# Kernel tuning notes

Measured on AMD Instinct MI355X. Metric: run time of the kernel, lower is better.

## Reference

```python
import jax, jax.numpy as jnp
import numpy as np

TEMPERATURE = 0.1
NEGATIVE_WEIGHT = 1.0
NORM_EPS = 1e-12  # matches torch F.normalize clamp_min eps


def setup_inputs() -> dict:
    key = jax.random.key(0)
    x = jax.random.normal(key, (8, 128, 16, 8, 8), dtype=jnp.float32)
    return {"x": x}


def reference(x):
    B, F, T, H, W = x.shape
    # transpose(0,1).flatten(1).transpose(0,1): (B,F,T,H,W) -> (N, F), N = B*T*H*W
    feats = jnp.transpose(x, (1, 0, 2, 3, 4)).reshape(F, -1).T  # [N, F]
    norms = jnp.maximum(jnp.linalg.norm(feats, axis=1, keepdims=True), NORM_EPS)
    x_norm = feats / norms  # unit vectors, [N, F]
    sims = (x_norm @ x_norm.T) / TEMPERATURE  # [N, N] cosine similarities
    n = sims.shape[0]
    # masked_select(~eye) + logsumexp == logsumexp with diagonal set to -inf
    sims = jnp.where(jnp.eye(n, dtype=bool), -jnp.inf, sims)
    diversity_loss = jax.nn.logsumexp(sims)
    return NEGATIVE_WEIGHT * diversity_loss
```

## Files before the change

kernel.cpp:

```cpp
#include <hip/hip_runtime.h>
#include <hip/hip_fp8.h>
#include <math.h>


#define NTILE 8256
#define NPBLK 1376

typedef __attribute__((ext_vector_type(4))) float f32x4;

#if __has_builtin(__builtin_amdgcn_exp2f)
#define EXP2F(x) __builtin_amdgcn_exp2f(x)
#else
#define EXP2F(x) exp2f(x)
#endif

__device__ inline unsigned int pk_fp8(float f0, float f1, float f2, float f3) {
#if __has_builtin(__builtin_amdgcn_cvt_pk_fp8_f32)
    unsigned int r = 0;
    r = __builtin_amdgcn_cvt_pk_fp8_f32(f0, f1, r, false);
    r = __builtin_amdgcn_cvt_pk_fp8_f32(f2, f3, r, true);
    return r;
#else
    union { unsigned char b[4]; unsigned int u; } v;
    v.b[0] = __hip_fp8_e4m3(f0).__x; v.b[1] = __hip_fp8_e4m3(f1).__x;
    v.b[2] = __hip_fp8_e4m3(f2).__x; v.b[3] = __hip_fp8_e4m3(f3).__x;
    return v.u;
#endif
}

__global__ __launch_bounds__(256)
void normalize_kernel(const float* __restrict__ x, unsigned char* __restrict__ Xs) {
    __shared__ float ldsf[128][33];
    __shared__ float ssred[8][32];
    __shared__ float invs[32];
    const int tid = threadIdx.x;
    const int b  = blockIdx.x >> 5;
    const int r0 = (blockIdx.x & 31) * 32;
    const int rl = tid & 31, fp = tid >> 5;
    const float* px = x + b * 131072 + r0 + rl;
    float ss = 0.f;
#pragma unroll
    for (int j = 0; j < 16; ++j) {
        int f = fp * 16 + j;
        float v = px[f * 1024];
        ldsf[f][rl] = v;
        ss = fmaf(v, v, ss);
    }
    ssred[fp][rl] = ss;
    __syncthreads();
    if (tid < 32) {
        float s = 0.f;
#pragma unroll
        for (int k = 0; k < 8; ++k) s += ssred[k][tid];
        invs[tid] = 1.0f / fmaxf(sqrtf(s), 1e-12f);
    }
    __syncthreads();
    {
        const int c   = tid;
        const int rgl = c >> 7;
        const int cc  = c & 127;
        const int t8  = (cc >> 6) & 1, q = (cc >> 4) & 3, r = cc & 15;
        const int row = rgl * 16 + r;
        const float inv = invs[row];
        union { unsigned int w[4]; int4 v; } u;
#pragma unroll
        for (int half = 0; half < 2; ++half) {
            const int k0 = t8 * 64 + half * 32 + q * 8;
            u.w[half * 2 + 0] = pk_fp8(ldsf[k0 + 0][row] * inv, ldsf[k0 + 1][row] * inv,
                                       ldsf[k0 + 2][row] * inv, ldsf[k0 + 3][row] * inv);
            u.w[half * 2 + 1] = pk_fp8(ldsf[k0 + 4][row] * inv, ldsf[k0 + 5][row] * inv,
                                       ldsf[k0 + 6][row] * inv, ldsf[k0 + 7][row] * inv);
        }
        const int rgg = blockIdx.x * 2 + rgl;
        ((int4*)Xs)[rgg * 128 + cc] = u.v;
    }
}

__global__ __launch_bounds__(256, 4)
void gram_lse_kernel(const int4* __restrict__ Xs, float* __restrict__ partials) {
    const int bk = blockIdx.x;
    const int tid = threadIdx.x;
    const int lane = tid & 63, w = tid >> 6;
    const int ga = (w & 1) * 2;
    const int gb = (w >> 1) * 2;
    const int quad = lane >> 4, colL = lane & 15;
    const float C = 14.426950408889634f;

    int L = bk * 6, I0 = 0;
    while (L >= 128 - I0) { L -= 128 - I0; ++I0; }
    int Is[6], Js[6];
    {
        int ii = I0, jj = I0 + L;
#pragma unroll
        for (int s = 0; s < 6; ++s) {
            Is[s] = ii; Js[s] = jj;
            if (++jj == 128) { ++ii; jj = ii; }
        }
    }

    int4 av[2][2];
    int IcurA = Is[0];
#pragma unroll
    for (int g = 0; g < 2; ++g)
#pragma unroll
        for (int t8 = 0; t8 < 2; ++t8)
            av[g][t8] = Xs[(Is[0] * 4 + ga + g) * 128 + t8 * 64 + lane];

    int4 bv[3][2][2];
#pragma unroll
    for (int pf = 0; pf < 2; ++pf)
#pragma unroll
        for (int g = 0; g < 2; ++g)
#pragma unroll
            for (int t8 = 0; t8 < 2; ++t8)
                bv[pf][g][t8] = Xs[(Js[pf] * 4 + gb + g) * 128 + t8 * 64 + lane];

    float wsum = 0.f;
#pragma unroll
    for (int s = 0; s < 6; ++s) {
        if (s + 2 < 6) {
#pragma unroll
            for (int g = 0; g < 2; ++g)
#pragma unroll
                for (int t8 = 0; t8 < 2; ++t8)
                    bv[(s + 2) % 3][g][t8] =
                        Xs[(Js[s + 2] * 4 + gb + g) * 128 + t8 * 64 + lane];
        }
        if (Is[s] != IcurA) {
#pragma unroll
            for (int g = 0; g < 2; ++g)
#pragma unroll
                for (int t8 = 0; t8 < 2; ++t8)
                    av[g][t8] = Xs[(Is[s] * 4 + ga + g) * 128 + t8 * 64 + lane];
            IcurA = Is[s];
        }

        f32x4 acc[2][2];
#pragma unroll
        for (int i = 0; i < 2; ++i)
#pragma unroll
            for (int j = 0; j < 2; ++j) acc[i][j] = (f32x4){0.f, 0.f, 0.f, 0.f};
#pragma unroll
        for (int t = 0; t < 4; ++t) {
            long aL[2], bL[2];
#pragma unroll
            for (int g = 0; g < 2; ++g) {
                aL[g] = ((const long*)&av[g][t >> 1])[t & 1];
                bL[g] = ((const long*)&bv[s % 3][g][t >> 1])[t & 1];
            }
#pragma unroll
            for (int i = 0; i < 2; ++i)
#pragma unroll
                for (int j = 0; j < 2; ++j)
                    acc[i][j] = __builtin_amdgcn_mfma_f32_16x16x32_fp8_fp8(
                        aL[i], bL[j], acc[i][j], 0, 0, 0);
        }

        const bool diagT = (Is[s] == Js[s]);
        float lsum = 0.f;
#pragma unroll
        for (int i = 0; i < 2; ++i) {
            const int rbase = (ga + i) * 16 + quad * 4;
#pragma unroll
            for (int j = 0; j < 2; ++j) {
                const int cbase = (gb + j) * 16 + colL;
#pragma unroll
                for (int g = 0; g < 4; ++g) {
                    if (diagT && (rbase + g == cbase)) continue;
                    lsum += EXP2F(fmaf(C, acc[i][j][g], -C));
                }
            }
        }
        wsum += diagT ? lsum : 2.0f * lsum;
    }

#pragma unroll
    for (int o = 32; o > 0; o >>= 1) wsum += __shfl_down(wsum, o, 64);
    __shared__ float red[4];
    if (lane == 0) red[w] = wsum;
    __syncthreads();
    if (tid == 0) partials[bk] = red[0] + red[1] + red[2] + red[3];
}

__global__ __launch_bounds__(256)
void final_kernel(const float* __restrict__ partials, float* __restrict__ out) {
    double s = 0.0;
    for (int i = threadIdx.x; i < NPBLK; i += 256) s += (double)partials[i];
#pragma unroll
    for (int o = 32; o > 0; o >>= 1) s += __shfl_down(s, o, 64);
    __shared__ double red[4];
    if ((threadIdx.x & 63) == 0) red[threadIdx.x >> 6] = s;
    __syncthreads();
    if (threadIdx.x == 0)
        out[0] = (float)(10.0 + log(red[0] + red[1] + red[2] + red[3]));
}

extern "C" void kernel_launch(void* const* d_in, const int* in_sizes, int n_in,
                              void* d_out, int out_size, void* d_ws, size_t ws_size,
                              hipStream_t stream) {
    const float* x = (const float*)d_in[0];
    float* out = (float*)d_out;
    float* partials = (float*)d_ws;
    unsigned char* Xs = (unsigned char*)d_ws + 131072;

    normalize_kernel<<<256, 256, 0, stream>>>(x, Xs);
    gram_lse_kernel<<<NPBLK, 256, 0, stream>>>((const int4*)Xs, partials);
    final_kernel<<<1, 256, 0, stream>>>(partials, out);
}
```

Baseline: 72.06 us.

## Fuse final reduction into gram kernel via last-block atomic counter and rebalance tiles

```diff
diff --git a/kernel.cpp b/kernel.cpp
--- a/kernel.cpp
+++ b/kernel.cpp
@@ -4,7 +4,7 @@
 
 
 #define NTILE 8256
-#define NPBLK 1376
+#define NPBLK 1024
 
 typedef __attribute__((ext_vector_type(4))) float f32x4;
 
@@ -29,7 +29,9 @@
 }
 
 __global__ __launch_bounds__(256)
-void normalize_kernel(const float* __restrict__ x, unsigned char* __restrict__ Xs) {
+void normalize_kernel(const float* __restrict__ x, unsigned char* __restrict__ Xs,
+                      unsigned int* __restrict__ counter) {
+    if (blockIdx.x == 0 && threadIdx.x == 0) counter[0] = 0u;
     __shared__ float ldsf[128][33];
     __shared__ float ssred[8][32];
     __shared__ float invs[32];
@@ -76,25 +78,26 @@
     }
 }
 
-__global__ __launch_bounds__(256, 4)
-void gram_lse_kernel(const int4* __restrict__ Xs, float* __restrict__ partials) {
-    const int bk = blockIdx.x;
-    const int tid = threadIdx.x;
-    const int lane = tid & 63, w = tid >> 6;
+template <int NT>
+__device__ __forceinline__ float gram_tiles(const int4* __restrict__ Xs,
+                                            int tstart, int lane, int w) {
     const int ga = (w & 1) * 2;
     const int gb = (w >> 1) * 2;
     const int quad = lane >> 4, colL = lane & 15;
     const float C = 14.426950408889634f;
 
-    int L = bk * 6, I0 = 0;
-    while (L >= 128 - I0) { L -= 128 - I0; ++I0; }
-    int Is[6], Js[6];
+    int Is[NT], Js[NT];
     {
-        int ii = I0, jj = I0 + L;
-#pragma unroll
-        for (int s = 0; s < 6; ++s) {
-            Is[s] = ii; Js[s] = jj;
-            if (++jj == 128) { ++ii; jj = ii; }
+        const int t = tstart;
+        int i = (int)((257.0 - sqrt(66049.0 - 8.0 * (double)t)) * 0.5);
+        if (i < 0) i = 0;
+        while ((((i + 1) * (256 - i)) >> 1) <= t) ++i;
+        while (((i * (257 - i)) >> 1) > t) --i;
+        int j = i + (t - ((i * (257 - i)) >> 1));
+#pragma unroll
+        for (int s = 0; s < NT; ++s) {
+            Is[s] = i; Js[s] = j;
+            if (++j == 128) { ++i; j = i; }
         }
     }
 
@@ -117,8 +120,8 @@
 
     float wsum = 0.f;
 #pragma unroll
-    for (int s = 0; s < 6; ++s) {
-        if (s + 2 < 6) {
+    for (int s = 0; s < NT; ++s) {
+        if (s + 2 < NT) {
 #pragma unroll
             for (int g = 0; g < 2; ++g)
 #pragma unroll
@@ -157,42 +160,63 @@
         }
 
         const bool diagT = (Is[s] == Js[s]);
-        float lsum = 0.f;
+        float l0 = 0.f, l1 = 0.f;
 #pragma unroll
         for (int i = 0; i < 2; ++i) {
             const int rbase = (ga + i) * 16 + quad * 4;
+            float lacc = 0.f;
 #pragma unroll
             for (int j = 0; j < 2; ++j) {
                 const int cbase = (gb + j) * 16 + colL;
 #pragma unroll
                 for (int g = 0; g < 4; ++g) {
                     if (diagT && (rbase + g == cbase)) continue;
-                    lsum += EXP2F(fmaf(C, acc[i][j][g], -C));
+                    lacc += EXP2F(fmaf(C, acc[i][j][g], -C));
                 }
             }
-        }
+            if (i == 0) l0 = lacc; else l1 = lacc;
+        }
+        const float lsum = l0 + l1;
         wsum += diagT ? lsum : 2.0f * lsum;
     }
+    return wsum;
+}
+
+__global__ __launch_bounds__(256, 4)
+void gram_lse_kernel(const int4* __restrict__ Xs, float* __restrict__ partials,
+                     unsigned int* __restrict__ counter, float* __restrict__ out) {
+    const int bk = blockIdx.x;
+    const int tid = threadIdx.x;
+    const int lane = tid & 63, w = tid >> 6;
+    const int tstart = bk * 8 + (bk < 64 ? bk : 64);
+
+    float wsum = (bk < 64) ? gram_tiles<9>(Xs, tstart, lane, w)
+                           : gram_tiles<8>(Xs, tstart, lane, w);
 
 #pragma unroll
     for (int o = 32; o > 0; o >>= 1) wsum += __shfl_down(wsum, o, 64);
     __shared__ float red[4];
+    __shared__ bool last;
     if (lane == 0) red[w] = wsum;
     __syncthreads();
-    if (tid == 0) partials[bk] = red[0] + red[1] + red[2] + red[3];
-}
-
-__global__ __launch_bounds__(256)
-void final_kernel(const float* __restrict__ partials, float* __restrict__ out) {
-    double s = 0.0;
-    for (int i = threadIdx.x; i < NPBLK; i += 256) s += (double)partials[i];
-#pragma unroll
-    for (int o = 32; o > 0; o >>= 1) s += __shfl_down(s, o, 64);
-    __shared__ double red[4];
-    if ((threadIdx.x & 63) == 0) red[threadIdx.x >> 6] = s;
-    __syncthreads();
-    if (threadIdx.x == 0)
-        out[0] = (float)(10.0 + log(red[0] + red[1] + red[2] + red[3]));
+    if (tid == 0) {
+        partials[bk] = red[0] + red[1] + red[2] + red[3];
+        __threadfence();
+        last = (atomicAdd(counter, 1u) == NPBLK - 1);
+    }
+    __syncthreads();
+    if (last) {
+        __threadfence();
+        double s = 0.0;
+        for (int i = tid; i < NPBLK; i += 256) s += (double)partials[i];
+#pragma unroll
+        for (int o = 32; o > 0; o >>= 1) s += __shfl_down(s, o, 64);
+        __shared__ double dred[4];
+        if (lane == 0) dred[w] = s;
+        __syncthreads();
+        if (tid == 0)
+            out[0] = (float)(10.0 + log(dred[0] + dred[1] + dred[2] + dred[3]));
+    }
 }
 
 extern "C" void kernel_launch(void* const* d_in, const int* in_sizes, int n_in,
@@ -201,9 +225,9 @@
     const float* x = (const float*)d_in[0];
     float* out = (float*)d_out;
     float* partials = (float*)d_ws;
+    unsigned int* counter = (unsigned int*)((char*)d_ws + 4096);
     unsigned char* Xs = (unsigned char*)d_ws + 131072;
 
-    normalize_kernel<<<256, 256, 0, stream>>>(x, Xs);
-    gram_lse_kernel<<<NPBLK, 256, 0, stream>>>((const int4*)Xs, partials);
-    final_kernel<<<1, 256, 0, stream>>>(partials, out);
-}
+    normalize_kernel<<<256, 256, 0, stream>>>(x, Xs, counter);
+    gram_lse_kernel<<<NPBLK, 256, 0, stream>>>((const int4*)Xs, partials, counter, out);
+}
```

Measured after the change: 109.5 us. 1.52x slower.
